# Performance work log

Measured on AMD Instinct MI355X. Metric: run time of the kernel, lower is better.

The kernel has to match this reference:

```python
import jax, jax.numpy as jnp
import numpy as np

N_NODES = 100000
N_EDGES = 1600000
IN_DIM = 64
HID_DIM = 32


def setup_inputs() -> dict:
    key = jax.random.key(0)
    k1, k2, k3, k4 = jax.random.split(key, 4)
    features = jax.random.normal(k1, (N_NODES, IN_DIM), dtype=jnp.float32)
    src = jax.random.randint(k2, (N_EDGES,), 0, N_NODES, dtype=jnp.int32)
    dst = jax.random.randint(k3, (N_EDGES,), 0, N_NODES, dtype=jnp.int32)
    # Glorot-uniform weight as in DGL GraphConv reset_parameters
    limit = (6.0 / (IN_DIM + HID_DIM)) ** 0.5
    W = jax.random.uniform(k4, (IN_DIM, HID_DIM), dtype=jnp.float32,
                           minval=-limit, maxval=limit)
    b = jnp.zeros((HID_DIM,), dtype=jnp.float32)
    return {"features": features, "src": src, "dst": dst, "W": W, "b": b}


def reference(features, src, dst, W, b):
    """DGL GraphConv(norm='both', activation=relu):
    out = relu(D_in^{-1/2} A D_out^{-1/2} (X W) + b)
    (weight applied first since in_dim > out_dim)."""
    n = features.shape[0]
    ones = jnp.ones(src.shape[0], dtype=features.dtype)
    deg_out = jax.ops.segment_sum(ones, src, num_segments=n)  # out-degree
    deg_in = jax.ops.segment_sum(ones, dst, num_segments=n)   # in-degree
    norm_src = jnp.clip(deg_out, 1.0, None) ** -0.5          # [N]
    norm_dst = jnp.clip(deg_in, 1.0, None) ** -0.5           # [N]

    h = (features @ W) * norm_src[:, None]                    # [N, hid]
    msg = h[src]                                              # [E, hid] gather
    agg = jax.ops.segment_sum(msg, dst, num_segments=n)       # [N, hid] scatter-add
    out = agg * norm_dst[:, None] + b
    return jax.nn.relu(out)
```

## Files before the change

### kernel.cpp

```cpp
#include <hip/hip_runtime.h>
#include <hip/hip_fp16.h>

#define IN_DIM 64
#define HID 32
#define SHIFT 8
#define BKEYS 256
#define CAP 4608
#define HCAP 2560
#define CHUNK 4096
#define MAXB 512

__global__ void zero_kernel(unsigned* __restrict__ p) {
    p[threadIdx.x + blockIdx.x * 256] = 0u;
}

__global__ __launch_bounds__(512) void multisplit_kernel(
    const int* __restrict__ src, const int* __restrict__ dst, int E, int NB,
    unsigned* __restrict__ gcur_d, unsigned* __restrict__ gcur_s,
    unsigned* __restrict__ bkt_pairs, unsigned char* __restrict__ bkt_srcs)
{
    __shared__ unsigned hist_d[MAXB], cur_d[MAXB], gb_d[MAXB];
    __shared__ unsigned hist_s[MAXB], cur_s[MAXB], gb_s[MAXB];
    int t = threadIdx.x;
    int e0 = blockIdx.x * CHUNK;
    int cnt = min(CHUNK, E - e0);
    hist_d[t] = 0; hist_s[t] = 0; cur_d[t] = 0; cur_s[t] = 0;
    __syncthreads();
    int n4 = cnt >> 2;
    const int4* s4 = (const int4*)(src + e0);
    const int4* d4 = (const int4*)(dst + e0);
    int4 sa = make_int4(-1, -1, -1, -1), da = sa, sb = sa, db = sa;
    if (t < n4)       { sa = s4[t];       da = d4[t]; }
    if (t + 512 < n4) { sb = s4[t + 512]; db = d4[t + 512]; }
    int sc = -1, dc = -1;
    int ti = (n4 << 2) + t;
    if (t < (cnt & 3)) { sc = src[e0 + ti]; dc = dst[e0 + ti]; }
    if (da.x >= 0) { atomicAdd(&hist_d[da.x >> SHIFT], 1u); atomicAdd(&hist_s[sa.x >> SHIFT], 1u);
                     atomicAdd(&hist_d[da.y >> SHIFT], 1u); atomicAdd(&hist_s[sa.y >> SHIFT], 1u);
                     atomicAdd(&hist_d[da.z >> SHIFT], 1u); atomicAdd(&hist_s[sa.z >> SHIFT], 1u);
                     atomicAdd(&hist_d[da.w >> SHIFT], 1u); atomicAdd(&hist_s[sa.w >> SHIFT], 1u); }
    if (db.x >= 0) { atomicAdd(&hist_d[db.x >> SHIFT], 1u); atomicAdd(&hist_s[sb.x >> SHIFT], 1u);
                     atomicAdd(&hist_d[db.y >> SHIFT], 1u); atomicAdd(&hist_s[sb.y >> SHIFT], 1u);
                     atomicAdd(&hist_d[db.z >> SHIFT], 1u); atomicAdd(&hist_s[sb.z >> SHIFT], 1u);
                     atomicAdd(&hist_d[db.w >> SHIFT], 1u); atomicAdd(&hist_s[sb.w >> SHIFT], 1u); }
    if (dc >= 0)   { atomicAdd(&hist_d[dc >> SHIFT], 1u);   atomicAdd(&hist_s[sc >> SHIFT], 1u); }
    __syncthreads();
    if (t < NB) {
        unsigned hd = hist_d[t], hs = hist_s[t];
        if (hd) gb_d[t] = atomicAdd(&gcur_d[t], hd);
        if (hs) gb_s[t] = atomicAdd(&gcur_s[t], hs);
    }
    __syncthreads();
    int dv[9] = {da.x, da.y, da.z, da.w, db.x, db.y, db.z, db.w, dc};
    int sv[9] = {sa.x, sa.y, sa.z, sa.w, sb.x, sb.y, sb.z, sb.w, sc};
#pragma unroll
    for (int j = 0; j < 9; ++j) {
        if (dv[j] < 0) continue;
        int kd = dv[j] >> SHIFT;
        unsigned pos = gb_d[kd] + atomicAdd(&cur_d[kd], 1u);
        if (pos < CAP)
            bkt_pairs[(size_t)kd * CAP + pos] =
                (((unsigned)dv[j] & (BKEYS - 1)) << 17) | (unsigned)sv[j];
        int ks = sv[j] >> SHIFT;
        unsigned pos2 = gb_s[ks] + atomicAdd(&cur_s[ks], 1u);
        if (pos2 < CAP)
            bkt_srcs[(size_t)ks * CAP + pos2] = (unsigned char)(sv[j] & (BKEYS - 1));
    }
}

__global__ __launch_bounds__(512) void degxw_kernel(
    const unsigned char* __restrict__ bkt_srcs, const unsigned* __restrict__ gcur_s,
    const float* __restrict__ X, const float* __restrict__ W,
    int N, unsigned short* __restrict__ h16)
{
    __shared__ float Ws[IN_DIM * HID];
    __shared__ unsigned cnt[128];
    __shared__ float nrm[128];
    int t = threadIdx.x;
    int blk = blockIdx.x, bin = blk >> 1;
    unsigned half = blk & 1;
    ((float4*)Ws)[t] = ((const float4*)W)[t];
    if (t < 128) cnt[t] = 0;
    __syncthreads();
    unsigned m = gcur_s[bin];
    if (m > CAP) m = CAP;
    const unsigned char* bs = bkt_srcs + (size_t)bin * CAP;
    const uchar4* bs4 = (const uchar4*)bs;
    unsigned m4 = m >> 2;
    for (unsigned i = t; i < m4; i += 512) {
        uchar4 kk = bs4[i];
        if ((kk.x >> 7) == half) atomicAdd(&cnt[kk.x & 127], 1u);
        if ((kk.y >> 7) == half) atomicAdd(&cnt[kk.y & 127], 1u);
        if ((kk.z >> 7) == half) atomicAdd(&cnt[kk.z & 127], 1u);
        if ((kk.w >> 7) == half) atomicAdd(&cnt[kk.w & 127], 1u);
    }
    for (unsigned i = (m4 << 2) + t; i < m; i += 512) {
        unsigned k = bs[i];
        if ((k >> 7) == half) atomicAdd(&cnt[k & 127], 1u);
    }
    __syncthreads();
    if (t < 128) nrm[t] = rsqrtf(fmaxf((float)cnt[t], 1.0f));
    __syncthreads();
    int q = t & 7, ln = t >> 3;
#pragma unroll
    for (int pass = 0; pass < 2; ++pass) {
        int lv = pass * 64 + ln;
        int v = bin * BKEYS + (int)half * 128 + lv;
        if (v < N) {
            const float4* Xr = (const float4*)(X + (size_t)v * IN_DIM);
            float4 acc = make_float4(0.f, 0.f, 0.f, 0.f);
#pragma unroll
            for (int kk = 0; kk < 16; ++kk) {
                float4 xv = Xr[kk];
                int k0 = kk * 4;
                float4 w0 = ((float4*)Ws)[(k0 + 0) * 8 + q];
                float4 w1 = ((float4*)Ws)[(k0 + 1) * 8 + q];
                float4 w2 = ((float4*)Ws)[(k0 + 2) * 8 + q];
                float4 w3 = ((float4*)Ws)[(k0 + 3) * 8 + q];
                acc.x += xv.x * w0.x + xv.y * w1.x + xv.z * w2.x + xv.w * w3.x;
                acc.y += xv.x * w0.y + xv.y * w1.y + xv.z * w2.y + xv.w * w3.y;
                acc.z += xv.x * w0.z + xv.y * w1.z + xv.z * w2.z + xv.w * w3.z;
                acc.w += xv.x * w0.w + xv.y * w1.w + xv.z * w2.w + xv.w * w3.w;
            }
            float s = nrm[lv];
            __half2 a  = __floats2half2_rn(acc.x * s, acc.y * s);
            __half2 b2 = __floats2half2_rn(acc.z * s, acc.w * s);
            uint2 u;
            u.x = *(unsigned*)&a;
            u.y = *(unsigned*)&b2;
            ((uint2*)h16)[(size_t)v * 8 + q] = u;
        }
    }
}

__global__ __launch_bounds__(512) void csrgather_kernel(
    const unsigned* __restrict__ bkt_pairs, const unsigned* __restrict__ gcur_d,
    const unsigned short* __restrict__ h16, const float* __restrict__ bias,
    float* __restrict__ out, int N)
{
    __shared__ unsigned cnt[128], ex[128], cur[128];
    __shared__ unsigned ecsr[HCAP];
    int t = threadIdx.x;
    int blk = blockIdx.x, bin = blk >> 1;
    unsigned half = blk & 1;
    if (t < 128) { cnt[t] = 0; cur[t] = 0; }
    __syncthreads();
    unsigned m = gcur_d[bin];
    if (m > CAP) m = CAP;
    const unsigned* bp = bkt_pairs + (size_t)bin * CAP;
    for (unsigned i = t; i < m; i += 512) {
        unsigned k = bp[i] >> 17;
        if ((k >> 7) == half) atomicAdd(&cnt[k & 127], 1u);
    }
    __syncthreads();
    if (t < 128) ex[t] = cnt[t];
    __syncthreads();
    for (int off = 1; off < 128; off <<= 1) {
        unsigned u = (t >= off && t < 128) ? ex[t - off] : 0;
        __syncthreads();
        if (t < 128) ex[t] += u;
        __syncthreads();
    }
    for (unsigned i = t; i < m; i += 512) {
        unsigned p = bp[i];
        unsigned k = p >> 17;
        if ((k >> 7) == half) {
            unsigned kk = k & 127;
            unsigned pos = (ex[kk] - cnt[kk]) + atomicAdd(&cur[kk], 1u);
            if (pos < HCAP) ecsr[pos] = p & 0x1FFFFu;
        }
    }
    __syncthreads();
    int lane = t & 63, w = t >> 6;
    int hsel = lane >> 5, slot = (lane >> 2) & 7, q = lane & 3;
    float4 bq0 = ((const float4*)bias)[q * 2];
    float4 bq1 = ((const float4*)bias)[q * 2 + 1];
#pragma unroll 2
    for (int j = 0; j < 8; ++j) {
        int lv = w * 16 + j * 2 + hsel;
        unsigned dg = cnt[lv];
        unsigned st = ex[lv] - dg;
        unsigned en = st + dg; if (en > HCAP) en = HCAP;
        float a0=0.f,a1=0.f,a2=0.f,a3=0.f,a4=0.f,a5=0.f,a6=0.f,a7=0.f;
        unsigned u = st + slot;
        for (; u + 8 < en; u += 16) {
            unsigned s0 = ecsr[u];
            unsigned s1 = ecsr[u + 8];
            uint4 hv0 = ((const uint4*)h16)[(size_t)s0 * 4 + q];
            uint4 hv1 = ((const uint4*)h16)[(size_t)s1 * 4 + q];
            __half2* hp0 = (__half2*)&hv0;
            __half2* hp1 = (__half2*)&hv1;
            float2 f0 = __half22float2(hp0[0]), g0 = __half22float2(hp1[0]);
            float2 f1 = __half22float2(hp0[1]), g1 = __half22float2(hp1[1]);
            float2 f2 = __half22float2(hp0[2]), g2 = __half22float2(hp1[2]);
            float2 f3 = __half22float2(hp0[3]), g3 = __half22float2(hp1[3]);
            a0 += f0.x + g0.x; a1 += f0.y + g0.y;
            a2 += f1.x + g1.x; a3 += f1.y + g1.y;
            a4 += f2.x + g2.x; a5 += f2.y + g2.y;
            a6 += f3.x + g3.x; a7 += f3.y + g3.y;
        }
        if (u < en) {
            unsigned s = ecsr[u];
            uint4 hv = ((const uint4*)h16)[(size_t)s * 4 + q];
            __half2* hp = (__half2*)&hv;
            float2 f0 = __half22float2(hp[0]);
            float2 f1 = __half22float2(hp[1]);
            float2 f2 = __half22float2(hp[2]);
            float2 f3 = __half22float2(hp[3]);
            a0 += f0.x; a1 += f0.y; a2 += f1.x; a3 += f1.y;
            a4 += f2.x; a5 += f2.y; a6 += f3.x; a7 += f3.y;
        }
#pragma unroll
        for (int off = 4; off <= 16; off <<= 1) {
            a0 += __shfl_xor(a0, off, 64); a1 += __shfl_xor(a1, off, 64);
            a2 += __shfl_xor(a2, off, 64); a3 += __shfl_xor(a3, off, 64);
            a4 += __shfl_xor(a4, off, 64); a5 += __shfl_xor(a5, off, 64);
            a6 += __shfl_xor(a6, off, 64); a7 += __shfl_xor(a7, off, 64);
        }
        int v = bin * BKEYS + (int)half * 128 + lv;
        if (slot == 0 && v < N) {
            float nv = rsqrtf(fmaxf((float)dg, 1.0f));
            float4 o0, o1;
            o0.x = fmaxf(a0 * nv + bq0.x, 0.f);
            o0.y = fmaxf(a1 * nv + bq0.y, 0.f);
            o0.z = fmaxf(a2 * nv + bq0.z, 0.f);
            o0.w = fmaxf(a3 * nv + bq0.w, 0.f);
            o1.x = fmaxf(a4 * nv + bq1.x, 0.f);
            o1.y = fmaxf(a5 * nv + bq1.y, 0.f);
            o1.z = fmaxf(a6 * nv + bq1.z, 0.f);
            o1.w = fmaxf(a7 * nv + bq1.w, 0.f);
            float* op = out + (size_t)v * HID + q * 8;
            *(float4*)op = o0;
            *(float4*)(op + 4) = o1;
        }
    }
}

extern "C" void kernel_launch(void* const* d_in, const int* in_sizes, int n_in,
                              void* d_out, int out_size, void* d_ws, size_t ws_size,
                              hipStream_t stream) {
    const float* X   = (const float*)d_in[0];
    const int*   src = (const int*)d_in[1];
    const int*   dst = (const int*)d_in[2];
    const float* W   = (const float*)d_in[3];
    const float* b   = (const float*)d_in[4];
    float* out = (float*)d_out;

    int N = in_sizes[0] / IN_DIM;
    int E = in_sizes[1];
    int NB = (N + BKEYS - 1) / BKEYS;

    unsigned* gcur_d = (unsigned*)d_ws;
    unsigned* gcur_s = gcur_d + MAXB;
    unsigned* bkt_pairs = gcur_s + MAXB;
    unsigned char* bkt_srcs = (unsigned char*)(bkt_pairs + (size_t)NB * CAP);
    unsigned short* h16 = (unsigned short*)(bkt_srcs + (size_t)NB * CAP);

    zero_kernel<<<4, 256, 0, stream>>>(gcur_d);
    multisplit_kernel<<<(E + CHUNK - 1) / CHUNK, 512, 0, stream>>>(
        src, dst, E, NB, gcur_d, gcur_s, bkt_pairs, bkt_srcs);
    degxw_kernel<<<NB * 2, 512, 0, stream>>>(bkt_srcs, gcur_s, X, W, N, h16);
    csrgather_kernel<<<NB * 2, 512, 0, stream>>>(bkt_pairs, gcur_d, h16, b, out, N);
}
```

Baseline: 151.4 us.

## Assign one node per 4-lane group in aggregation instead of 8 slots per node

The per-node aggregation changes its thread mapping. Previously 8 edge slots × 4 quarter-rows per node, looping over 8 node pairs per wave with a shuffle reduction. Now each group of 4 lanes owns one node and walks all of its edges serially with 4-way unrolling. This removes the cross-lane shuffle reduction, the outer node loop and the idle slots on low-degree nodes. The cost is serial per-lane edge loops and more lane divergence when degrees vary within a wave.

```diff
diff --git a/kernel.cpp b/kernel.cpp
--- a/kernel.cpp
+++ b/kernel.cpp
@@ -172,67 +172,73 @@
     }
     __syncthreads();
     int lane = t & 63, w = t >> 6;
-    int hsel = lane >> 5, slot = (lane >> 2) & 7, q = lane & 3;
-    float4 bq0 = ((const float4*)bias)[q * 2];
-    float4 bq1 = ((const float4*)bias)[q * 2 + 1];
-#pragma unroll 2
-    for (int j = 0; j < 8; ++j) {
-        int lv = w * 16 + j * 2 + hsel;
-        unsigned dg = cnt[lv];
-        unsigned st = ex[lv] - dg;
-        unsigned en = st + dg; if (en > HCAP) en = HCAP;
-        float a0=0.f,a1=0.f,a2=0.f,a3=0.f,a4=0.f,a5=0.f,a6=0.f,a7=0.f;
-        unsigned u = st + slot;
-        for (; u + 8 < en; u += 16) {
-            unsigned s0 = ecsr[u];
-            unsigned s1 = ecsr[u + 8];
-            uint4 hv0 = ((const uint4*)h16)[(size_t)s0 * 4 + q];
-            uint4 hv1 = ((const uint4*)h16)[(size_t)s1 * 4 + q];
-            __half2* hp0 = (__half2*)&hv0;
-            __half2* hp1 = (__half2*)&hv1;
-            float2 f0 = __half22float2(hp0[0]), g0 = __half22float2(hp1[0]);
-            float2 f1 = __half22float2(hp0[1]), g1 = __half22float2(hp1[1]);
-            float2 f2 = __half22float2(hp0[2]), g2 = __half22float2(hp1[2]);
-            float2 f3 = __half22float2(hp0[3]), g3 = __half22float2(hp1[3]);
-            a0 += f0.x + g0.x; a1 += f0.y + g0.y;
-            a2 += f1.x + g1.x; a3 += f1.y + g1.y;
-            a4 += f2.x + g2.x; a5 += f2.y + g2.y;
-            a6 += f3.x + g3.x; a7 += f3.y + g3.y;
-        }
-        if (u < en) {
-            unsigned s = ecsr[u];
-            uint4 hv = ((const uint4*)h16)[(size_t)s * 4 + q];
-            __half2* hp = (__half2*)&hv;
-            float2 f0 = __half22float2(hp[0]);
-            float2 f1 = __half22float2(hp[1]);
-            float2 f2 = __half22float2(hp[2]);
-            float2 f3 = __half22float2(hp[3]);
-            a0 += f0.x; a1 += f0.y; a2 += f1.x; a3 += f1.y;
-            a4 += f2.x; a5 += f2.y; a6 += f3.x; a7 += f3.y;
-        }
-#pragma unroll
-        for (int off = 4; off <= 16; off <<= 1) {
-            a0 += __shfl_xor(a0, off, 64); a1 += __shfl_xor(a1, off, 64);
-            a2 += __shfl_xor(a2, off, 64); a3 += __shfl_xor(a3, off, 64);
-            a4 += __shfl_xor(a4, off, 64); a5 += __shfl_xor(a5, off, 64);
-            a6 += __shfl_xor(a6, off, 64); a7 += __shfl_xor(a7, off, 64);
-        }
-        int v = bin * BKEYS + (int)half * 128 + lv;
-        if (slot == 0 && v < N) {
-            float nv = rsqrtf(fmaxf((float)dg, 1.0f));
-            float4 o0, o1;
-            o0.x = fmaxf(a0 * nv + bq0.x, 0.f);
-            o0.y = fmaxf(a1 * nv + bq0.y, 0.f);
-            o0.z = fmaxf(a2 * nv + bq0.z, 0.f);
-            o0.w = fmaxf(a3 * nv + bq0.w, 0.f);
-            o1.x = fmaxf(a4 * nv + bq1.x, 0.f);
-            o1.y = fmaxf(a5 * nv + bq1.y, 0.f);
-            o1.z = fmaxf(a6 * nv + bq1.z, 0.f);
-            o1.w = fmaxf(a7 * nv + bq1.w, 0.f);
-            float* op = out + (size_t)v * HID + q * 8;
-            *(float4*)op = o0;
-            *(float4*)(op + 4) = o1;
-        }
+    int n16 = lane >> 2;
+    int q = lane & 3;
+    int lv = w * 16 + n16;
+    unsigned dg = cnt[lv];
+    unsigned en = ex[lv]; if (en > HCAP) en = HCAP;
+    unsigned st = ex[lv] - dg; if (st > en) st = en;
+    unsigned len = en - st;
+    const uint4* h16q = (const uint4*)h16;
+
+    float a0=0.f,a1=0.f,a2=0.f,a3=0.f,a4=0.f,a5=0.f,a6=0.f,a7=0.f;
+    unsigned i = 0;
+    for (; i + 4 <= len; i += 4) {
+        unsigned s0 = ecsr[st + i];
+        unsigned s1 = ecsr[st + i + 1];
+        unsigned s2 = ecsr[st + i + 2];
+        unsigned s3 = ecsr[st + i + 3];
+        uint4 h0 = h16q[(size_t)s0 * 4 + q];
+        uint4 h1 = h16q[(size_t)s1 * 4 + q];
+        uint4 h2 = h16q[(size_t)s2 * 4 + q];
+        uint4 h3 = h16q[(size_t)s3 * 4 + q];
+        __half2* p0 = (__half2*)&h0;  __half2* p1 = (__half2*)&h1;
+        __half2* p2 = (__half2*)&h2;  __half2* p3 = (__half2*)&h3;
+        float2 f;
+        f = __half22float2(p0[0]); a0 += f.x; a1 += f.y;
+        f = __half22float2(p0[1]); a2 += f.x; a3 += f.y;
+        f = __half22float2(p0[2]); a4 += f.x; a5 += f.y;
+        f = __half22float2(p0[3]); a6 += f.x; a7 += f.y;
+        f = __half22float2(p1[0]); a0 += f.x; a1 += f.y;
+        f = __half22float2(p1[1]); a2 += f.x; a3 += f.y;
+        f = __half22float2(p1[2]); a4 += f.x; a5 += f.y;
+        f = __half22float2(p1[3]); a6 += f.x; a7 += f.y;
+        f = __half22float2(p2[0]); a0 += f.x; a1 += f.y;
+        f = __half22float2(p2[1]); a2 += f.x; a3 += f.y;
+        f = __half22float2(p2[2]); a4 += f.x; a5 += f.y;
+        f = __half22float2(p2[3]); a6 += f.x; a7 += f.y;
+        f = __half22float2(p3[0]); a0 += f.x; a1 += f.y;
+        f = __half22float2(p3[1]); a2 += f.x; a3 += f.y;
+        f = __half22float2(p3[2]); a4 += f.x; a5 += f.y;
+        f = __half22float2(p3[3]); a6 += f.x; a7 += f.y;
+    }
+    for (; i < len; ++i) {
+        unsigned s = ecsr[st + i];
+        uint4 hv = h16q[(size_t)s * 4 + q];
+        __half2* hp = (__half2*)&hv;
+        float2 f;
+        f = __half22float2(hp[0]); a0 += f.x; a1 += f.y;
+        f = __half22float2(hp[1]); a2 += f.x; a3 += f.y;
+        f = __half22float2(hp[2]); a4 += f.x; a5 += f.y;
+        f = __half22float2(hp[3]); a6 += f.x; a7 += f.y;
+    }
+    int v = bin * BKEYS + (int)half * 128 + lv;
+    if (v < N) {
+        float nv = rsqrtf(fmaxf((float)dg, 1.0f));
+        float4 bq0 = ((const float4*)bias)[q * 2];
+        float4 bq1 = ((const float4*)bias)[q * 2 + 1];
+        float4 o0, o1;
+        o0.x = fmaxf(a0 * nv + bq0.x, 0.f);
+        o0.y = fmaxf(a1 * nv + bq0.y, 0.f);
+        o0.z = fmaxf(a2 * nv + bq0.z, 0.f);
+        o0.w = fmaxf(a3 * nv + bq0.w, 0.f);
+        o1.x = fmaxf(a4 * nv + bq1.x, 0.f);
+        o1.y = fmaxf(a5 * nv + bq1.y, 0.f);
+        o1.z = fmaxf(a6 * nv + bq1.z, 0.f);
+        o1.w = fmaxf(a7 * nv + bq1.w, 0.f);
+        float* op = out + (size_t)v * HID + q * 8;
+        *(float4*)op = o0;
+        *(float4*)(op + 4) = o1;
     }
 }
 
```

Result: faster. 145.9 us (-3.6%).
